# Performance work log

Hardware: AMD Instinct MI355X
Metric: run time of the kernel (lower is better)

The kernel has to match this reference:

```python
import jax, jax.numpy as jnp
import numpy as np

B, N, FD, D, HF, WF = 4, 6, 256, 128, 64, 120
IMG_H, IMG_W = 480, 960
EPS_LN = 1e-5


def bilinear_sample(fmap, pts):
    """fmap: (B,C,H,W); pts: (B,P,2) xy pixel coords. Returns (B,P,C) values
    (zeros padding, align_corners=True convention) and (B,P) in-bounds mask."""
    Bc, C, H, W = fmap.shape
    flat = fmap.reshape(Bc, C, H * W)
    x, y = pts[..., 0], pts[..., 1]
    x0, y0 = jnp.floor(x), jnp.floor(y)
    out = jnp.zeros((Bc, pts.shape[1], C), fmap.dtype)
    for dx in (0.0, 1.0):
        for dy in (0.0, 1.0):
            cx, cy = x0 + dx, y0 + dy
            wgt = (1.0 - jnp.abs(x - cx)) * (1.0 - jnp.abs(y - cy))
            inb = (cx >= 0) & (cx <= W - 1) & (cy >= 0) & (cy <= H - 1)
            idx = (jnp.clip(cy, 0, H - 1) * W + jnp.clip(cx, 0, W - 1)).astype(jnp.int32)
            g = jnp.take_along_axis(flat, idx[:, None, :], axis=2)  # (B,C,P)
            out = out + (g * (wgt * inb)[:, None, :]).transpose(0, 2, 1)
    valid = (x >= 0) & (x <= W - 1) & (y >= 0) & (y <= H - 1)
    return out, valid


def _l2norm(x, axis):
    n = jnp.sqrt(jnp.sum(x * x, axis=axis, keepdims=True))
    return x / jnp.maximum(n, 1e-12)


def _ln(x, g, b):
    mu = jnp.mean(x, axis=-1, keepdims=True)
    var = jnp.mean((x - mu) ** 2, axis=-1, keepdims=True)
    return (x - mu) / jnp.sqrt(var + EPS_LN) * g + b


def setup_inputs() -> dict:
    key = jax.random.key(0)
    ks = jax.random.split(key, 12)
    rng = np.random.RandomState(0)
    feature = jax.random.normal(ks[0], (B, N, FD, HF, WF), jnp.float32)
    # realistic intrinsics (same K family for src/tar so homographies land in-frame)
    K = np.zeros((B, N, 3, 3), np.float32)
    K[..., 0, 0] = IMG_W * 0.8 * (1 + 0.01 * rng.randn(B, N))
    K[..., 1, 1] = IMG_W * 0.8 * (1 + 0.01 * rng.randn(B, N))
    K[..., 0, 2] = IMG_W / 2
    K[..., 1, 2] = IMG_H / 2
    K[..., 2, 2] = 1.0
    I_tar_inv = np.linalg.inv(K[:, 0]).astype(np.float32)  # (B,3,3)
    # extrinsics: near-identity rotation + small translation
    E = np.tile(np.eye(4, dtype=np.float32), (B, N, 1, 1))
    w = 0.02 * rng.randn(B, N, 3).astype(np.float32)
    skew = np.zeros((B, N, 3, 3), np.float32)
    skew[..., 0, 1], skew[..., 0, 2] = -w[..., 2], w[..., 1]
    skew[..., 1, 0], skew[..., 1, 2] = w[..., 2], -w[..., 0]
    skew[..., 2, 0], skew[..., 2, 1] = -w[..., 1], w[..., 0]
    E[..., :3, :3] = np.eye(3, dtype=np.float32) + skew
    E[..., :3, 3] = 0.1 * rng.randn(B, N, 3).astype(np.float32)
    nv = np.tile(np.array([0.0, -1.0, 0.0], np.float32), (B, 1, 1))
    nv += 0.01 * rng.randn(B, 1, 3).astype(np.float32)
    nv /= np.linalg.norm(nv, axis=-1, keepdims=True)
    sc_in, sc_hid = 1.0 / np.sqrt(FD), 1.0 / np.sqrt(D)
    return {
        "feature": feature,
        "I_src": jnp.asarray(K),
        "I_tar_inv": jnp.asarray(I_tar_inv),
        "E": jnp.asarray(E),
        "dis": jnp.float32(1.5),
        "norm_vec": jnp.asarray(nv),
        "bn_gamma": jnp.ones((FD,), jnp.float32),
        "bn_beta": jnp.zeros((FD,), jnp.float32),
        "bn_mean": jnp.zeros((FD,), jnp.float32),
        "bn_var": jnp.ones((FD,), jnp.float32),
        "conv_w": jax.random.normal(ks[1], (D, FD), jnp.float32) * sc_in,
        "ln1_g": jnp.ones((D,), jnp.float32),
        "ln1_b": jnp.zeros((D,), jnp.float32),
        "mlp_w1": jax.random.normal(ks[2], (D, 2 * D), jnp.float32) * sc_hid,
        "mlp_b1": jnp.zeros((2 * D,), jnp.float32),
        "mlp_w2": jax.random.normal(ks[3], (2 * D, D), jnp.float32) * sc_hid,
        "mlp_b2": jnp.zeros((D,), jnp.float32),
        "ln2_g": jnp.ones((D,), jnp.float32),
        "ln2_b": jnp.zeros((D,), jnp.float32),
    }


def reference(feature, I_src, I_tar_inv, E, dis, norm_vec, bn_gamma, bn_beta,
              bn_mean, bn_var, conv_w, ln1_g, ln1_b, mlp_w1, mlp_b1, mlp_w2,
              mlp_b2, ln2_g, ln2_b):
    b, n, fd, h, w = feature.shape
    d = conv_w.shape[0]
    P = h * w
    # feature_linear: BN (inference stats) + ReLU + 1x1 conv (no bias)
    f = (feature - bn_mean[:, None, None]) / jnp.sqrt(bn_var[:, None, None] + 1e-5)
    f = f * bn_gamma[:, None, None] + bn_beta[:, None, None]
    f = jax.nn.relu(f)
    val = jnp.einsum('of,bnfhw->bnohw', conv_w, f)  # (b,n,d,h,w)
    # homography of normalized grid scaled to image pixels
    xs = jnp.linspace(0.0, 1.0, w)
    ys = jnp.linspace(0.0, 1.0, h)
    X, Y = jnp.meshgrid(xs, ys)  # (h,w), xy indexing
    pix = jnp.stack([X.ravel() * IMG_W, Y.ravel() * IMG_H, jnp.ones(P)], 0)  # (3,P)
    R = E[..., :3, :3]
    T = E[..., :3, 3:]
    Hm = I_src @ (R - (T @ norm_vec[:, None]) / dis) @ I_tar_inv[:, None]  # (b,n,3,3)
    homo = jnp.einsum('bnij,jp->bnip', Hm, pix.astype(Hm.dtype))
    uv = homo[:, :, :2] / homo[:, :, 2:3]
    uv = uv / jnp.array([[IMG_W], [IMG_H]], uv.dtype)  # (b,n,2,P) in ~[0,1]
    # HomoGuideAttention
    pts = (uv * jnp.array([[w], [h]], uv.dtype)).transpose(0, 1, 3, 2).reshape(b * n, P, 2)
    sampled, valid = bilinear_sample(val.reshape(b * n, d, h, w), pts)  # (bn,P,d),(bn,P)
    keyv = _l2norm(sampled, axis=2).reshape(b, n, P, d)
    query = val[:, 0]  # (b,d,h,w)
    q = _l2norm(query.reshape(b, d, P), axis=1)
    dot = jnp.einsum('bdp,bnpd->bnp', q, keyv)
    dot = dot * valid.reshape(b, n, P).astype(dot.dtype)
    att = jax.nn.softmax(dot, axis=1)
    z = jnp.einsum('bnp,bnpd->bpd', att, sampled.reshape(b, n, P, d))
    z = z.transpose(0, 2, 1).reshape(b, d, h, w) + query
    z = z.reshape(b, d, P).transpose(0, 2, 1)  # (b,P,d)
    z = _ln(z, ln1_g, ln1_b)
    hmid = jax.nn.gelu(z @ mlp_w1 + mlp_b1, approximate=False)
    z = z + (hmid @ mlp_w2 + mlp_b2)
    z = _ln(z, ln2_g, ln2_b)
    return z.transpose(0, 2, 1).reshape(b, d, h, w)
```

## Files before the change

### kernel.cpp

```cpp
#include <hip/hip_runtime.h>
#include <hip/hip_bf16.h>
#include <math.h>

#define B_ 4
#define N_ 6
#define FD_ 256
#define D_ 128
#define HF_ 64
#define WF_ 120
#define P_ (HF_*WF_)

typedef __attribute__((ext_vector_type(8))) short short8;
typedef __attribute__((ext_vector_type(4))) float floatx4;
typedef __attribute__((ext_vector_type(4))) unsigned int uint4e;

__device__ inline float gred_sum(float v) {
  v += __shfl_xor(v, 1); v += __shfl_xor(v, 2);
  v += __shfl_xor(v, 4); v += __shfl_xor(v, 8);
  return v;
}

__device__ inline unsigned short f2bf(float f) {
  unsigned int u = __builtin_bit_cast(unsigned int, f);
  u += 0x7fffu + ((u >> 16) & 1u);
  return (unsigned short)(u >> 16);
}
__device__ inline float bf2f(unsigned short h) {
  return __builtin_bit_cast(float, ((unsigned int)h) << 16);
}

__global__ void prep_kernel(const float* __restrict__ I_src, const float* __restrict__ I_tar_inv,
                            const float* __restrict__ E, const float* __restrict__ dis,
                            const float* __restrict__ norm_vec,
                            const float* __restrict__ bn_gamma, const float* __restrict__ bn_beta,
                            const float* __restrict__ bn_mean, const float* __restrict__ bn_var,
                            float* __restrict__ bnscale, float* __restrict__ bnbias,
                            float* __restrict__ Hm) {
  int t = threadIdx.x;
  if (t < FD_) {
    float s = bn_gamma[t] * rsqrtf(bn_var[t] + 1e-5f);
    bnscale[t] = s;
    bnbias[t] = bn_beta[t] - bn_mean[t] * s;
  }
  if (t < B_*N_) {
    int b = t / N_;
    const float* e = E + t*16;
    const float* nv = norm_vec + b*3;
    float inv_dis = 1.0f / dis[0];
    float M[9];
    #pragma unroll
    for (int r = 0; r < 3; r++)
      #pragma unroll
      for (int c = 0; c < 3; c++)
        M[r*3+c] = e[r*4+c] - e[r*4+3]*nv[c]*inv_dis;
    const float* Is = I_src + t*9;
    float A[9];
    #pragma unroll
    for (int r = 0; r < 3; r++)
      #pragma unroll
      for (int c = 0; c < 3; c++)
        A[r*3+c] = Is[r*3+0]*M[0*3+c] + Is[r*3+1]*M[1*3+c] + Is[r*3+2]*M[2*3+c];
    const float* It = I_tar_inv + b*9;
    #pragma unroll
    for (int r = 0; r < 3; r++)
      #pragma unroll
      for (int c = 0; c < 3; c++)
        Hm[t*9 + r*3+c] = A[r*3+0]*It[0*3+c] + A[r*3+1]*It[1*3+c] + A[r*3+2]*It[2*3+c];
  }
}

__global__ void swizzle_w_kernel(const float* __restrict__ conv_w, unsigned short* __restrict__ wswz) {
  int t = blockIdx.x * 256 + threadIdx.x;
  int j    =  t        & 7;
  int lane = (t >> 3)  & 63;
  int dt   = (t >> 9)  & 7;
  int kc   =  t >> 12;
  int d = dt*16 + (lane & 15);
  int k = kc*32 + (lane >> 4)*8 + j;
  wswz[t] = f2bf(conv_w[d*FD_ + k]);
}

__global__ void swizzle_mlp_kernel(const float* __restrict__ w1, const float* __restrict__ w2,
                                   unsigned short* __restrict__ w1s, unsigned short* __restrict__ w2s) {
  int t = blockIdx.x * 256 + threadIdx.x;
  if (t < 32768) {
    int j    =  t        & 7;
    int lane = (t >> 3)  & 63;
    int dt   = (t >> 9)  & 15;
    int kc   =  t >> 13;
    int n = dt*16 + (lane & 15);
    int k = kc*32 + (lane >> 4)*8 + j;
    w1s[t] = f2bf(w1[k*256 + n]);
  } else {
    int u = t - 32768;
    int j    =  u        & 7;
    int lane = (u >> 3)  & 63;
    int dt   = (u >> 9)  & 7;
    int kc   =  u >> 12;
    int n = dt*16 + (lane & 15);
    int k = kc*32 + (lane >> 4)*8 + j;
    w2s[u] = f2bf(w2[k*128 + n]);
  }
}

__global__ __launch_bounds__(256) void conv_kernel(const float* __restrict__ feature,
    const unsigned short* __restrict__ wswz, const float* __restrict__ bnscale,
    const float* __restrict__ bnbias, float* __restrict__ val) {
  __shared__ float sbn[512];
  int tid = threadIdx.x;
  if (tid < 256) { sbn[tid] = bnscale[tid]; sbn[256+tid] = bnbias[tid]; }
  __syncthreads();

  int bn = blockIdx.y;
  int p0 = blockIdx.x * 64;
  int ln = tid & 63, wv = tid >> 6;
  int m = ln & 15, q = ln >> 4;
  const float* fbase = feature + (size_t)bn*FD_*P_ + p0 + wv*16 + m;

  floatx4 acc[8];
  #pragma unroll
  for (int dt = 0; dt < 8; dt++) acc[dt] = (floatx4){0.f,0.f,0.f,0.f};

  for (int kc = 0; kc < 8; kc++) {
    int kb = kc*32 + q*8;
    float xv[8];
    #pragma unroll
    for (int j = 0; j < 8; j++)
      xv[j] = fbase[(size_t)(kb + j)*P_];
    unsigned int pk[4];
    #pragma unroll
    for (int jj = 0; jj < 4; jj++) {
      float s0 = sbn[kb+2*jj],   b0 = sbn[256+kb+2*jj];
      float s1 = sbn[kb+2*jj+1], b1 = sbn[256+kb+2*jj+1];
      unsigned short h0 = f2bf(fmaxf(xv[2*jj]*s0+b0, 0.f));
      unsigned short h1 = f2bf(fmaxf(xv[2*jj+1]*s1+b1, 0.f));
      pk[jj] = (unsigned int)h0 | ((unsigned int)h1 << 16);
    }
    uint4e ua = {pk[0], pk[1], pk[2], pk[3]};
    short8 af = __builtin_bit_cast(short8, ua);
    #pragma unroll
    for (int dt = 0; dt < 8; dt++) {
      short8 bfg = *(const short8*)(wswz + (((size_t)kc*8 + dt)*64 + ln)*8);
      acc[dt] = __builtin_amdgcn_mfma_f32_16x16x32_bf16(af, bfg, acc[dt], 0, 0, 0);
    }
  }
  #pragma unroll
  for (int dt = 0; dt < 8; dt++) {
    #pragma unroll
    for (int r = 0; r < 4; r++) {
      int pp = p0 + wv*16 + q*4 + r;
      int d  = dt*16 + m;
      val[((size_t)bn*P_ + pp)*D_ + d] = acc[dt][r];
    }
  }
}

__global__ __launch_bounds__(256) void att_kernel(const float* __restrict__ val,
    const float* __restrict__ Hm, const float* __restrict__ ln1_g,
    const float* __restrict__ ln1_b, float* __restrict__ zbuf) {
  int b = blockIdx.y;
  int p0 = blockIdx.x * 32;
  int tid = threadIdx.x;
  int ln = tid & 63, wv = tid >> 6;
  int grp = ln >> 4, c = ln & 15;

  float g1[8], be1[8];
  *(float4*)&g1[0]  = *(const float4*)(ln1_g + c*8);
  *(float4*)&g1[4]  = *(const float4*)(ln1_g + c*8 + 4);
  *(float4*)&be1[0] = *(const float4*)(ln1_b + c*8);
  *(float4*)&be1[4] = *(const float4*)(ln1_b + c*8 + 4);

  for (int pi = 0; pi < 2; pi++) {
    int p = p0 + wv*8 + grp*2 + pi;
    int py = p / WF_, px = p - py*WF_;
    float pixx = (float)px * (960.f/119.f);
    float pixy = (float)py * (480.f/63.f);

    const float* qptr = val + ((size_t)(b*N_)*P_ + p)*D_ + c*8;
    float qv[8];
    *(float4*)&qv[0] = *(const float4*)qptr;
    *(float4*)&qv[4] = *(const float4*)(qptr + 4);
    float qp = 0.f;
    #pragma unroll
    for (int i = 0; i < 8; i++) qp += qv[i]*qv[i];
    float qinv = 1.f / fmaxf(sqrtf(gred_sum(qp)), 1e-12f);

    float dotv[N_];
    float sv[N_][8];
    #pragma unroll
    for (int n = 0; n < N_; n++) {
      const float* H = Hm + (b*N_+n)*9;
      float hx = H[0]*pixx + H[1]*pixy + H[2];
      float hy = H[3]*pixx + H[4]*pixy + H[5];
      float hz = H[6]*pixx + H[7]*pixy + H[8];
      float sx = (hx/hz) * ((float)WF_/960.f);
      float sy = (hy/hz) * ((float)HF_/480.f);
      float x0f = floorf(sx), y0f = floorf(sy);
      float fx = sx - x0f, fy = sy - y0f;
      int x0 = (int)x0f, y0 = (int)y0f;
      const float* base = val + ((size_t)(b*N_+n)*P_)*D_ + c*8;
      float acc[8];
      #pragma unroll
      for (int i = 0; i < 8; i++) acc[i] = 0.f;
      #pragma unroll
      for (int dy = 0; dy < 2; dy++) {
        #pragma unroll
        for (int dx = 0; dx < 2; dx++) {
          int cx = x0 + dx, cy = y0 + dy;
          float wgt = (dx ? fx : 1.f-fx) * (dy ? fy : 1.f-fy);
          bool inb = (cx >= 0) && (cx <= WF_-1) && (cy >= 0) && (cy <= HF_-1);
          int icx = min(max(cx,0),WF_-1), icy = min(max(cy,0),HF_-1);
          const float* gp = base + (size_t)(icy*WF_ + icx)*D_;
          float4 ga = *(const float4*)gp;
          float4 gb = *(const float4*)(gp + 4);
          float wm = inb ? wgt : 0.f;
          acc[0] += ga.x*wm; acc[1] += ga.y*wm; acc[2] += ga.z*wm; acc[3] += ga.w*wm;
          acc[4] += gb.x*wm; acc[5] += gb.y*wm; acc[6] += gb.z*wm; acc[7] += gb.w*wm;
        }
      }
      float ssp = 0.f, qsp = 0.f;
      #pragma unroll
      for (int i = 0; i < 8; i++) { ssp += acc[i]*acc[i]; qsp += qv[i]*acc[i]; }
      float ss = gred_sum(ssp);
      float qs = gred_sum(qsp);
      float dn = qs * qinv / fmaxf(sqrtf(ss), 1e-12f);
      bool valid = (sx >= 0.f) && (sx <= (float)(WF_-1)) && (sy >= 0.f) && (sy <= (float)(HF_-1));
      dotv[n] = valid ? dn : 0.f;
      #pragma unroll
      for (int i = 0; i < 8; i++) sv[n][i] = acc[i];
    }
    float mx = dotv[0];
    #pragma unroll
    for (int n = 1; n < N_; n++) mx = fmaxf(mx, dotv[n]);
    float e[N_]; float den = 0.f;
    #pragma unroll
    for (int n = 0; n < N_; n++) { e[n] = expf(dotv[n]-mx); den += e[n]; }
    float rden = 1.f/den;
    float z[8];
    #pragma unroll
    for (int i = 0; i < 8; i++) z[i] = qv[i];
    #pragma unroll
    for (int n = 0; n < N_; n++) {
      float a = e[n]*rden;
      #pragma unroll
      for (int i = 0; i < 8; i++) z[i] += a*sv[n][i];
    }
    float sp = 0.f;
    #pragma unroll
    for (int i = 0; i < 8; i++) sp += z[i];
    float mu = gred_sum(sp) * (1.f/128.f);
    float vp = 0.f;
    #pragma unroll
    for (int i = 0; i < 8; i++) { float d0 = z[i]-mu; vp += d0*d0; }
    float var = gred_sum(vp) * (1.f/128.f);
    float rs = rsqrtf(var + 1e-5f);
    float o[8];
    #pragma unroll
    for (int i = 0; i < 8; i++) o[i] = (z[i]-mu)*rs*g1[i] + be1[i];
    float* zp = zbuf + ((size_t)b*P_ + p)*D_ + c*8;
    *(float4*)zp       = *(float4*)&o[0];
    *(float4*)(zp + 4) = *(float4*)&o[4];
  }
}

__global__ __launch_bounds__(256) void mlp_kernel(const float* __restrict__ zbuf,
    const unsigned short* __restrict__ w1s, const float* __restrict__ b1,
    const unsigned short* __restrict__ w2s, const float* __restrict__ b2,
    const float* __restrict__ ln2_g, const float* __restrict__ ln2_b,
    float* __restrict__ out) {
  __shared__ unsigned short zt[64*136];
  __shared__ unsigned short ht[64*264];
  int tid = threadIdx.x;
  int b = blockIdx.y;
  int p0 = blockIdx.x * 64;

  #pragma unroll
  for (int i = 0; i < 8; i++) {
    int idx = tid + i*256;
    int pp = idx >> 5, dc = idx & 31;
    float4 v = *(const float4*)(zbuf + ((size_t)b*P_ + p0 + pp)*D_ + dc*4);
    ushort4 hh;
    hh.x = f2bf(v.x); hh.y = f2bf(v.y); hh.z = f2bf(v.z); hh.w = f2bf(v.w);
    *(ushort4*)&zt[pp*136 + dc*4] = hh;
  }
  __syncthreads();

  int ln = tid & 63, wv = tid >> 6;
  int m = ln & 15, q = ln >> 4;

  floatx4 a1[16];
  #pragma unroll
  for (int dt = 0; dt < 16; dt++) a1[dt] = (floatx4){0.f,0.f,0.f,0.f};
  #pragma unroll
  for (int kc = 0; kc < 4; kc++) {
    short8 af = *(const short8*)&zt[(wv*16+m)*136 + kc*32 + q*8];
    #pragma unroll
    for (int dt = 0; dt < 16; dt++) {
      short8 bfg = *(const short8*)(w1s + (((size_t)kc*16 + dt)*64 + ln)*8);
      a1[dt] = __builtin_amdgcn_mfma_f32_16x16x32_bf16(af, bfg, a1[dt], 0, 0, 0);
    }
  }
  #pragma unroll
  for (int dt = 0; dt < 16; dt++) {
    float bb = b1[dt*16 + m];
    #pragma unroll
    for (int r = 0; r < 4; r++) {
      float x = a1[dt][r] + bb;
      float hv = 0.5f*x*(1.f + erff(x*0.70710678118654752f));
      int pp = wv*16 + q*4 + r;
      ht[pp*264 + dt*16 + m] = f2bf(hv);
    }
  }
  __syncthreads();

  floatx4 a2[8];
  #pragma unroll
  for (int dt = 0; dt < 8; dt++) a2[dt] = (floatx4){0.f,0.f,0.f,0.f};
  #pragma unroll
  for (int kc = 0; kc < 8; kc++) {
    short8 af = *(const short8*)&ht[(wv*16+m)*264 + kc*32 + q*8];
    #pragma unroll
    for (int dt = 0; dt < 8; dt++) {
      short8 bfg = *(const short8*)(w2s + (((size_t)kc*8 + dt)*64 + ln)*8);
      a2[dt] = __builtin_amdgcn_mfma_f32_16x16x32_bf16(af, bfg, a2[dt], 0, 0, 0);
    }
  }
  float y[8][4];
  #pragma unroll
  for (int dt = 0; dt < 8; dt++) {
    float bb = b2[dt*16 + m];
    #pragma unroll
    for (int r = 0; r < 4; r++) {
      int pp = wv*16 + q*4 + r;
      y[dt][r] = a2[dt][r] + bb + bf2f(zt[pp*136 + dt*16 + m]);
    }
  }
  float gg[8], be[8];
  #pragma unroll
  for (int dt = 0; dt < 8; dt++) { gg[dt] = ln2_g[dt*16+m]; be[dt] = ln2_b[dt*16+m]; }
  #pragma unroll
  for (int r = 0; r < 4; r++) {
    float sp = 0.f;
    #pragma unroll
    for (int dt = 0; dt < 8; dt++) sp += y[dt][r];
    float mu = gred_sum(sp) * (1.f/128.f);
    float vp = 0.f;
    #pragma unroll
    for (int dt = 0; dt < 8; dt++) { float d0 = y[dt][r]-mu; vp += d0*d0; }
    float rs = rsqrtf(gred_sum(vp) * (1.f/128.f) + 1e-5f);
    #pragma unroll
    for (int dt = 0; dt < 8; dt++) y[dt][r] = (y[dt][r]-mu)*rs*gg[dt] + be[dt];
  }
  __syncthreads();
  float* yt = (float*)ht;
  #pragma unroll
  for (int dt = 0; dt < 8; dt++)
    #pragma unroll
    for (int r = 0; r < 4; r++)
      yt[(dt*16 + m)*66 + wv*16 + q*4 + r] = y[dt][r];
  __syncthreads();

  #pragma unroll
  for (int i = 0; i < 16; i++) {
    int idx = tid + i*256;
    int d = idx >> 5, f2 = idx & 31;
    float2 v = *(float2*)&yt[d*66 + f2*2];
    *(float2*)(out + ((size_t)(b*D_ + d))*P_ + p0 + f2*2) = v;
  }
}

extern "C" void kernel_launch(void* const* d_in, const int* in_sizes, int n_in,
                              void* d_out, int out_size, void* d_ws, size_t ws_size,
                              hipStream_t stream) {
  (void)in_sizes; (void)n_in; (void)out_size; (void)ws_size;
  const float* feature   = (const float*)d_in[0];
  const float* I_src     = (const float*)d_in[1];
  const float* I_tar_inv = (const float*)d_in[2];
  const float* E         = (const float*)d_in[3];
  const float* dis       = (const float*)d_in[4];
  const float* norm_vec  = (const float*)d_in[5];
  const float* bn_gamma  = (const float*)d_in[6];
  const float* bn_beta   = (const float*)d_in[7];
  const float* bn_mean   = (const float*)d_in[8];
  const float* bn_var    = (const float*)d_in[9];
  const float* conv_w    = (const float*)d_in[10];
  const float* ln1_g     = (const float*)d_in[11];
  const float* ln1_b     = (const float*)d_in[12];
  const float* mlp_w1    = (const float*)d_in[13];
  const float* mlp_b1    = (const float*)d_in[14];
  const float* mlp_w2    = (const float*)d_in[15];
  const float* mlp_b2    = (const float*)d_in[16];
  const float* ln2_g     = (const float*)d_in[17];
  const float* ln2_b     = (const float*)d_in[18];
  float* out = (float*)d_out;

  char* ws = (char*)d_ws;
  float* bnscale       = (float*)(ws + 0);
  float* bnbias        = (float*)(ws + 1024);
  float* Hm            = (float*)(ws + 2048);
  unsigned short* wswz = (unsigned short*)(ws + 4096);
  unsigned short* w1s  = (unsigned short*)(ws + 69632);
  unsigned short* w2s  = (unsigned short*)(ws + 135168);
  float* val  = (float*)(ws + 200704);
  float* zbuf = (float*)(ws + 200704 + 94371840ULL);

  hipLaunchKernelGGL(prep_kernel, dim3(1), dim3(256), 0, stream,
                     I_src, I_tar_inv, E, dis, norm_vec,
                     bn_gamma, bn_beta, bn_mean, bn_var, bnscale, bnbias, Hm);
  hipLaunchKernelGGL(swizzle_w_kernel, dim3(128), dim3(256), 0, stream, conv_w, wswz);
  hipLaunchKernelGGL(swizzle_mlp_kernel, dim3(256), dim3(256), 0, stream,
                     mlp_w1, mlp_w2, w1s, w2s);
  hipLaunchKernelGGL(conv_kernel, dim3(120, 24), dim3(256), 0, stream,
                     feature, wswz, bnscale, bnbias, val);
  hipLaunchKernelGGL(att_kernel, dim3(240, 4), dim3(256), 0, stream,
                     val, Hm, ln1_g, ln1_b, zbuf);
  hipLaunchKernelGGL(mlp_kernel, dim3(120, 4), dim3(256), 0, stream,
                     zbuf, w1s, mlp_b1, w2s, mlp_b2, ln2_g, ln2_b, out);
}
```

Baseline: 429.7 us.

## Store conv output and attention intermediate in bf16, stage conv inputs via LDS

The intermediate feature map `val` and the post-LN1 buffer `zbuf` are stored as bf16 instead of fp32, halving their memory traffic in conv, attention gather and MLP load. The conv kernel now loads the input with coalesced float4 reads into a double-buffered LDS tile, transposed for MFMA operands, instead of strided scalar loads. It also writes its output through an LDS tile for coalesced 16-byte stores. This adds bf16 rounding to the values used for the attention dot products and softmax, a small accuracy risk.

```diff
diff --git a/kernel.cpp b/kernel.cpp
--- a/kernel.cpp
+++ b/kernel.cpp
@@ -27,6 +27,10 @@
 }
 __device__ inline float bf2f(unsigned short h) {
   return __builtin_bit_cast(float, ((unsigned int)h) << 16);
+}
+__device__ inline void bfu2(unsigned int u, float& lo, float& hi) {
+  lo = __builtin_bit_cast(float, u << 16);
+  hi = __builtin_bit_cast(float, u & 0xffff0000u);
 }
 
 __global__ void prep_kernel(const float* __restrict__ I_src, const float* __restrict__ I_tar_inv,
@@ -105,59 +109,83 @@
 
 __global__ __launch_bounds__(256) void conv_kernel(const float* __restrict__ feature,
     const unsigned short* __restrict__ wswz, const float* __restrict__ bnscale,
-    const float* __restrict__ bnbias, float* __restrict__ val) {
+    const float* __restrict__ bnbias, unsigned short* __restrict__ val) {
+  __shared__ unsigned short apad[2][64*36];
+  __shared__ unsigned short ytile[64*136];
   __shared__ float sbn[512];
+
   int tid = threadIdx.x;
   if (tid < 256) { sbn[tid] = bnscale[tid]; sbn[256+tid] = bnbias[tid]; }
-  __syncthreads();
 
   int bn = blockIdx.y;
   int p0 = blockIdx.x * 64;
+  const float* fbase2 = feature + (size_t)bn*FD_*P_ + p0;
+
+  int K0 = tid >> 4;
+  int pc = tid & 15;
+  int sp = pc*4;
+
   int ln = tid & 63, wv = tid >> 6;
   int m = ln & 15, q = ln >> 4;
-  const float* fbase = feature + (size_t)bn*FD_*P_ + p0 + wv*16 + m;
+  int row = wv*16 + m;
+
+  auto stage = [&](int kc, int bb) {
+    int k0 = kc*32;
+    const float* fb = fbase2 + (size_t)(k0 + 2*K0)*P_ + sp;
+    float4 v0 = *(const float4*)fb;
+    float4 v1 = *(const float4*)(fb + P_);
+    float s0 = sbn[k0+2*K0],   b0 = sbn[256+k0+2*K0];
+    float s1 = sbn[k0+2*K0+1], b1 = sbn[256+k0+2*K0+1];
+    float a0[4] = {v0.x, v0.y, v0.z, v0.w};
+    float a1[4] = {v1.x, v1.y, v1.z, v1.w};
+    #pragma unroll
+    for (int i = 0; i < 4; i++) {
+      unsigned int w = (unsigned int)f2bf(fmaxf(a0[i]*s0+b0, 0.f))
+                     | ((unsigned int)f2bf(fmaxf(a1[i]*s1+b1, 0.f)) << 16);
+      *(unsigned int*)&apad[bb][(sp+i)*36 + 2*K0] = w;
+    }
+  };
 
   floatx4 acc[8];
   #pragma unroll
   for (int dt = 0; dt < 8; dt++) acc[dt] = (floatx4){0.f,0.f,0.f,0.f};
 
+  stage(0, 0);
+  __syncthreads();
+
   for (int kc = 0; kc < 8; kc++) {
-    int kb = kc*32 + q*8;
-    float xv[8];
-    #pragma unroll
-    for (int j = 0; j < 8; j++)
-      xv[j] = fbase[(size_t)(kb + j)*P_];
-    unsigned int pk[4];
-    #pragma unroll
-    for (int jj = 0; jj < 4; jj++) {
-      float s0 = sbn[kb+2*jj],   b0 = sbn[256+kb+2*jj];
-      float s1 = sbn[kb+2*jj+1], b1 = sbn[256+kb+2*jj+1];
-      unsigned short h0 = f2bf(fmaxf(xv[2*jj]*s0+b0, 0.f));
-      unsigned short h1 = f2bf(fmaxf(xv[2*jj+1]*s1+b1, 0.f));
-      pk[jj] = (unsigned int)h0 | ((unsigned int)h1 << 16);
-    }
-    uint4e ua = {pk[0], pk[1], pk[2], pk[3]};
+    int bb = kc & 1;
+    if (kc < 7) stage(kc+1, bb ^ 1);
+    uint2 u0 = *(const uint2*)&apad[bb][row*36 + q*8];
+    uint2 u1 = *(const uint2*)&apad[bb][row*36 + q*8 + 4];
+    uint4e ua = {u0.x, u0.y, u1.x, u1.y};
     short8 af = __builtin_bit_cast(short8, ua);
     #pragma unroll
     for (int dt = 0; dt < 8; dt++) {
       short8 bfg = *(const short8*)(wswz + (((size_t)kc*8 + dt)*64 + ln)*8);
       acc[dt] = __builtin_amdgcn_mfma_f32_16x16x32_bf16(af, bfg, acc[dt], 0, 0, 0);
     }
-  }
-  #pragma unroll
-  for (int dt = 0; dt < 8; dt++) {
-    #pragma unroll
-    for (int r = 0; r < 4; r++) {
-      int pp = p0 + wv*16 + q*4 + r;
-      int d  = dt*16 + m;
-      val[((size_t)bn*P_ + pp)*D_ + d] = acc[dt][r];
-    }
-  }
-}
-
-__global__ __launch_bounds__(256) void att_kernel(const float* __restrict__ val,
+    if (kc < 7) __syncthreads();
+  }
+
+  #pragma unroll
+  for (int dt = 0; dt < 8; dt++)
+    #pragma unroll
+    for (int r = 0; r < 4; r++)
+      ytile[(wv*16 + q*4 + r)*136 + dt*16 + m] = f2bf(acc[dt][r]);
+  __syncthreads();
+  #pragma unroll
+  for (int i = 0; i < 4; i++) {
+    int idx = tid + i*256;
+    int pp = idx >> 4, ch = idx & 15;
+    uint4 v = *(const uint4*)&ytile[pp*136 + ch*8];
+    *(uint4*)(val + ((size_t)bn*P_ + p0 + pp)*D_ + ch*8) = v;
+  }
+}
+
+__global__ __launch_bounds__(256) void att_kernel(const unsigned short* __restrict__ val,
     const float* __restrict__ Hm, const float* __restrict__ ln1_g,
-    const float* __restrict__ ln1_b, float* __restrict__ zbuf) {
+    const float* __restrict__ ln1_b, unsigned short* __restrict__ zbuf) {
   int b = blockIdx.y;
   int p0 = blockIdx.x * 32;
   int tid = threadIdx.x;
@@ -176,10 +204,11 @@
     float pixx = (float)px * (960.f/119.f);
     float pixy = (float)py * (480.f/63.f);
 
-    const float* qptr = val + ((size_t)(b*N_)*P_ + p)*D_ + c*8;
+    const unsigned short* qptr = val + ((size_t)(b*N_)*P_ + p)*D_ + c*8;
+    uint4 qu = *(const uint4*)qptr;
     float qv[8];
-    *(float4*)&qv[0] = *(const float4*)qptr;
-    *(float4*)&qv[4] = *(const float4*)(qptr + 4);
+    bfu2(qu.x, qv[0], qv[1]); bfu2(qu.y, qv[2], qv[3]);
+    bfu2(qu.z, qv[4], qv[5]); bfu2(qu.w, qv[6], qv[7]);
     float qp = 0.f;
     #pragma unroll
     for (int i = 0; i < 8; i++) qp += qv[i]*qv[i];
@@ -198,7 +227,7 @@
       float x0f = floorf(sx), y0f = floorf(sy);
       float fx = sx - x0f, fy = sy - y0f;
       int x0 = (int)x0f, y0 = (int)y0f;
-      const float* base = val + ((size_t)(b*N_+n)*P_)*D_ + c*8;
+      const unsigned short* base = val + ((size_t)(b*N_+n)*P_)*D_ + c*8;
       float acc[8];
       #pragma unroll
       for (int i = 0; i < 8; i++) acc[i] = 0.f;
@@ -210,12 +239,13 @@
           float wgt = (dx ? fx : 1.f-fx) * (dy ? fy : 1.f-fy);
           bool inb = (cx >= 0) && (cx <= WF_-1) && (cy >= 0) && (cy <= HF_-1);
           int icx = min(max(cx,0),WF_-1), icy = min(max(cy,0),HF_-1);
-          const float* gp = base + (size_t)(icy*WF_ + icx)*D_;
-          float4 ga = *(const float4*)gp;
-          float4 gb = *(const float4*)(gp + 4);
+          uint4 gu = *(const uint4*)(base + (size_t)(icy*WF_ + icx)*D_);
+          float g[8];
+          bfu2(gu.x, g[0], g[1]); bfu2(gu.y, g[2], g[3]);
+          bfu2(gu.z, g[4], g[5]); bfu2(gu.w, g[6], g[7]);
           float wm = inb ? wgt : 0.f;
-          acc[0] += ga.x*wm; acc[1] += ga.y*wm; acc[2] += ga.z*wm; acc[3] += ga.w*wm;
-          acc[4] += gb.x*wm; acc[5] += gb.y*wm; acc[6] += gb.z*wm; acc[7] += gb.w*wm;
+          #pragma unroll
+          for (int i = 0; i < 8; i++) acc[i] += g[i]*wm;
         }
       }
       float ssp = 0.f, qsp = 0.f;
@@ -254,16 +284,19 @@
     for (int i = 0; i < 8; i++) { float d0 = z[i]-mu; vp += d0*d0; }
     float var = gred_sum(vp) * (1.f/128.f);
     float rs = rsqrtf(var + 1e-5f);
-    float o[8];
-    #pragma unroll
-    for (int i = 0; i < 8; i++) o[i] = (z[i]-mu)*rs*g1[i] + be1[i];
-    float* zp = zbuf + ((size_t)b*P_ + p)*D_ + c*8;
-    *(float4*)zp       = *(float4*)&o[0];
-    *(float4*)(zp + 4) = *(float4*)&o[4];
-  }
-}
-
-__global__ __launch_bounds__(256) void mlp_kernel(const float* __restrict__ zbuf,
+    unsigned int ow[4];
+    #pragma unroll
+    for (int i = 0; i < 4; i++) {
+      float o0 = (z[2*i]-mu)*rs*g1[2*i] + be1[2*i];
+      float o1 = (z[2*i+1]-mu)*rs*g1[2*i+1] + be1[2*i+1];
+      ow[i] = (unsigned int)f2bf(o0) | ((unsigned int)f2bf(o1) << 16);
+    }
+    uint4 ov = make_uint4(ow[0], ow[1], ow[2], ow[3]);
+    *(uint4*)(zbuf + ((size_t)b*P_ + p)*D_ + c*8) = ov;
+  }
+}
+
+__global__ __launch_bounds__(256) void mlp_kernel(const unsigned short* __restrict__ zbuf,
     const unsigned short* __restrict__ w1s, const float* __restrict__ b1,
     const unsigned short* __restrict__ w2s, const float* __restrict__ b2,
     const float* __restrict__ ln2_g, const float* __restrict__ ln2_b,
@@ -275,13 +308,11 @@
   int p0 = blockIdx.x * 64;
 
   #pragma unroll
-  for (int i = 0; i < 8; i++) {
+  for (int i = 0; i < 4; i++) {
     int idx = tid + i*256;
-    int pp = idx >> 5, dc = idx & 31;
-    float4 v = *(const float4*)(zbuf + ((size_t)b*P_ + p0 + pp)*D_ + dc*4);
-    ushort4 hh;
-    hh.x = f2bf(v.x); hh.y = f2bf(v.y); hh.z = f2bf(v.z); hh.w = f2bf(v.w);
-    *(ushort4*)&zt[pp*136 + dc*4] = hh;
+    int pp = idx >> 4, ch = idx & 15;
+    uint4 v = *(const uint4*)(zbuf + ((size_t)b*P_ + p0 + pp)*D_ + ch*8);
+    *(uint4*)&zt[pp*136 + ch*8] = v;
   }
   __syncthreads();
 
@@ -401,8 +432,8 @@
   unsigned short* wswz = (unsigned short*)(ws + 4096);
   unsigned short* w1s  = (unsigned short*)(ws + 69632);
   unsigned short* w2s  = (unsigned short*)(ws + 135168);
-  float* val  = (float*)(ws + 200704);
-  float* zbuf = (float*)(ws + 200704 + 94371840ULL);
+  unsigned short* val  = (unsigned short*)(ws + 200704);
+  unsigned short* zbuf = (unsigned short*)(ws + 200704 + 47185920ULL);
 
   hipLaunchKernelGGL(prep_kernel, dim3(1), dim3(256), 0, stream,
                      I_src, I_tar_inv, E, dis, norm_vec,
```

Result: faster. 374.4 us (-12.9%).
